# Performance work log

Hardware: AMD Instinct MI355X
Metric: run time of the kernel (lower is better)

Reference implementation:

```python
import jax, jax.numpy as jnp
import numpy as np
import math

N, Tp1, V = 256, 33, 10000
D_FEAT, H, W_DIM = 1280, 512, 256
NULL_IDX = 0


def setup_inputs() -> dict:
    key = jax.random.key(0)
    ks = jax.random.split(key, 10)
    feats = jax.random.normal(ks[0], (N, D_FEAT, 4, 4), dtype=jnp.float32)
    captions = jax.random.randint(ks[1], (N, Tp1), 0, V)
    W_proj = jax.random.normal(ks[2], (D_FEAT, H), dtype=jnp.float32) / math.sqrt(D_FEAT)
    b_proj = jnp.zeros((H,), dtype=jnp.float32)
    W_embed = jax.random.normal(ks[3], (V, W_DIM), dtype=jnp.float32) / math.sqrt(V)
    Wx = jax.random.normal(ks[4], (W_DIM, 4 * H), dtype=jnp.float32) / math.sqrt(W_DIM)
    Wh = jax.random.normal(ks[5], (H, 4 * H), dtype=jnp.float32) / math.sqrt(H)
    Wattn = jax.random.normal(ks[6], (H, 4 * H), dtype=jnp.float32) / math.sqrt(H)
    b = jnp.zeros((4 * H,), dtype=jnp.float32)
    W_vocab = jax.random.normal(ks[7], (H, V), dtype=jnp.float32) / math.sqrt(H)
    b_vocab = jnp.zeros((V,), dtype=jnp.float32)
    return {"feats": feats, "captions": captions, "W_proj": W_proj, "b_proj": b_proj,
            "W_embed": W_embed, "Wx": Wx, "Wh": Wh, "Wattn": Wattn, "b": b,
            "W_vocab": W_vocab, "b_vocab": b_vocab}


def _attention_lstm(x, A_flat, h0, Wx, Wh, Wattn, b):
    # x: (N,T,W), A_flat: (N,H,16), h0: (N,H)
    Hh = h0.shape[1]
    scale = 1.0 / math.sqrt(Hh)

    def step(carry, x_t):
        h, c = carry
        # scaled dot-product attention over the 16 spatial positions
        scores = jnp.einsum('nh,nhp->np', h, A_flat) * scale       # (N,16)
        w = jax.nn.softmax(scores, axis=1)
        attn = jnp.einsum('nhp,np->nh', A_flat, w)                 # (N,H)
        a = x_t @ Wx + h @ Wh + b + attn @ Wattn                   # (N,4H)
        i = jax.nn.sigmoid(a[:, 0:Hh])
        f = jax.nn.sigmoid(a[:, Hh:2 * Hh])
        o = jax.nn.sigmoid(a[:, 2 * Hh:3 * Hh])
        g = jnp.tanh(a[:, 3 * Hh:4 * Hh])
        c_next = f * c + i * g
        h_next = o * jnp.tanh(c_next)
        return (h_next, c_next), h_next

    (_, _), hs = jax.lax.scan(step, (h0, h0), jnp.swapaxes(x, 0, 1))
    return jnp.swapaxes(hs, 0, 1)  # (N,T,H)


def reference(feats, captions, W_proj, b_proj, W_embed, Wx, Wh, Wattn, b, W_vocab, b_vocab):
    cap_in = captions[:, :-1]   # (N,T)
    cap_out = captions[:, 1:]   # (N,T)
    # project CNN features per spatial location: (N,Dfeat,4,4) -> (N,H,4,4)
    A = jnp.einsum('ncij,ch->nhij', feats, W_proj) + b_proj[None, :, None, None]
    h0 = A.mean(axis=(2, 3))                     # (N,H); c0 = h0
    A_flat = A.reshape(A.shape[0], A.shape[1], 16)
    x = W_embed[cap_in]                           # (N,T,W)
    h = _attention_lstm(x, A_flat, h0, Wx, Wh, Wattn, b)
    scores = jnp.einsum('nth,hv->ntv', h, W_vocab) + b_vocab   # (N,T,V)
    # temporal softmax loss, sum over tokens (ignoring NULL), averaged over N
    logp = jax.nn.log_softmax(scores, axis=-1)
    nll = -jnp.take_along_axis(logp, cap_out[..., None], axis=-1)[..., 0]  # (N,T)
    mask = (cap_out != NULL_IDX).astype(scores.dtype)
    loss = jnp.sum(nll * mask) / scores.shape[0]
    return loss
```

## Files before the change

### kernel.cpp

```cpp
#include <hip/hip_runtime.h>
#include <hip/hip_bf16.h>

#define NB   256
#define NT   32
#define NV   10000
#define NVP  10240
#define NDF  1280
#define NH   512
#define VT_N 40

typedef short bf16x8 __attribute__((ext_vector_type(8)));
typedef float f32x4  __attribute__((ext_vector_type(4)));
typedef unsigned short u16;

__device__ __forceinline__ float b2f(u16 u) {
    union { unsigned i; float f; } v; v.i = ((unsigned)u) << 16; return v.f;
}
__device__ __forceinline__ u16 f2b(float f) {
    union { float f; unsigned i; } v; v.f = f;
    unsigned r = v.i + 0x7FFF + ((v.i >> 16) & 1);
    return (u16)(r >> 16);
}

__device__ __forceinline__ void gload16(const u16* g, u16* l) {
    __builtin_amdgcn_global_load_lds(
        (const __attribute__((address_space(1))) void*)g,
        (__attribute__((address_space(3))) void*)l, 16, 0, 0);
}

static const size_t B_C     = 0;
static const size_t B_SCP   = B_C     + (size_t)256*512*4;
static const size_t B_PMAX  = B_SCP   + (size_t)2*32*256*16*4;
static const size_t B_PSUM  = B_PMAX  + (size_t)8192*VT_N*4;
static const size_t B_TGT   = B_PSUM  + (size_t)8192*VT_N*4;
static const size_t B_LOSS  = B_TGT   + (size_t)8192*4;
static const size_t B_AB    = B_LOSS  + 16;
static const size_t B_XPB   = B_AB    + (size_t)256*16*512*2;
static const size_t B_HALLB = B_XPB   + (size_t)32*256*2048*2;
static const size_t B_WVT   = B_HALLB + (size_t)32*256*512*2;
static const size_t B_WXT   = B_WVT   + (size_t)10240*512*2;
static const size_t B_WHAT  = B_WXT   + (size_t)2048*256*2;
static const size_t B_HB0   = B_WHAT  + (size_t)2048*1024*2;
static const size_t B_HB1   = B_HB0   + (size_t)256*512*2;
static const size_t B_PREAW = B_HB1   + (size_t)256*512*2;

__global__ __launch_bounds__(256) void tconv_kernel(
    const float* __restrict__ src, u16* __restrict__ dst,
    int K, int N, int Npad, int ldK, int koff)
{
    __shared__ u16 tile[64][65];
    const int k0 = blockIdx.y * 64, n0 = blockIdx.x * 64, tid = threadIdx.x;
#pragma unroll
    for (int i = 0; i < 16; i++) {
        int idx = tid + i * 256;
        int kk = idx >> 6, nn = idx & 63;
        int n = n0 + nn;
        float v = (n < N) ? src[(size_t)(k0 + kk) * N + n] : 0.f;
        tile[kk][nn] = f2b(v);
    }
    __syncthreads();
#pragma unroll
    for (int i = 0; i < 16; i++) {
        int idx = tid + i * 256;
        int nn = idx >> 6, kk = idx & 63;
        int n = n0 + nn;
        if (n < Npad) dst[(size_t)n * ldK + koff + k0 + kk] = tile[kk][nn];
    }
}

__global__ __launch_bounds__(256) void ftrans_kernel(
    const float* __restrict__ feats, u16* __restrict__ fT)
{
    const int cch = blockIdx.x, n = blockIdx.y, tid = threadIdx.x;
    __shared__ u16 lt[64][17];
    const int c0 = cch * 64;
    const int c = tid >> 2, p4 = (tid & 3) * 4;
    float4 v = *(const float4*)(feats + (size_t)n * 20480 + (size_t)(c0 + c) * 16 + p4);
    lt[c][p4] = f2b(v.x); lt[c][p4 + 1] = f2b(v.y);
    lt[c][p4 + 2] = f2b(v.z); lt[c][p4 + 3] = f2b(v.w);
    __syncthreads();
    const int p = tid >> 4, cg = tid & 15;
    ushort4 o;
    o.x = lt[cg * 4 + 0][p]; o.y = lt[cg * 4 + 1][p];
    o.z = lt[cg * 4 + 2][p]; o.w = lt[cg * 4 + 3][p];
    *(ushort4*)(fT + (size_t)(n * 16 + p) * 1280 + c0 + cg * 4) = o;
}

__global__ __launch_bounds__(256) void proj_gemm_kernel(
    const u16* __restrict__ fT, const u16* __restrict__ WpT,
    const float* __restrict__ bp, u16* __restrict__ Ab)
{
    const int rt = blockIdx.x;
    const int tid = threadIdx.x, w = tid >> 6, lane = tid & 63;
    const int r0 = rt * 64;
    const int lm = lane & 15, lkq = lane >> 4, lk = lkq * 8;
    const int nbase = w * 128;

    f32x4 acc[4][8];
#pragma unroll
    for (int mt = 0; mt < 4; mt++)
#pragma unroll
        for (int nt = 0; nt < 8; nt++) acc[mt][nt] = (f32x4){0.f, 0.f, 0.f, 0.f};

    for (int kc = 0; kc < 1280; kc += 32) {
        bf16x8 af[4];
#pragma unroll
        for (int mt = 0; mt < 4; mt++)
            af[mt] = *(const bf16x8*)(fT + (size_t)(r0 + mt * 16 + lm) * 1280 + kc + lk);
#pragma unroll
        for (int nt = 0; nt < 8; nt++) {
            bf16x8 bfg = *(const bf16x8*)(WpT + (size_t)(nbase + nt * 16 + lm) * 1280 + kc + lk);
#pragma unroll
            for (int mt = 0; mt < 4; mt++)
                acc[mt][nt] = __builtin_amdgcn_mfma_f32_16x16x32_bf16(af[mt], bfg, acc[mt][nt], 0, 0, 0);
        }
    }
    float bbv[8];
#pragma unroll
    for (int nt = 0; nt < 8; nt++) bbv[nt] = bp[nbase + nt * 16 + lm];
#pragma unroll
    for (int mt = 0; mt < 4; mt++)
#pragma unroll
        for (int nt = 0; nt < 8; nt++)
#pragma unroll
            for (int r = 0; r < 4; r++) {
                int row = r0 + mt * 16 + lkq * 4 + r;
                int col = nbase + nt * 16 + lm;
                Ab[(size_t)row * 512 + col] = f2b(acc[mt][nt][r] + bbv[nt]);
            }
}

__global__ __launch_bounds__(256) void projmean_kernel(
    const u16* __restrict__ Ab, float* __restrict__ c0, u16* __restrict__ hb0)
{
    const int n = blockIdx.x, tid = threadIdx.x;
    const int col0 = tid, col1 = tid + 256;
    float s0 = 0.f, s1 = 0.f;
#pragma unroll
    for (int p = 0; p < 16; p++) {
        const u16* ap = Ab + ((size_t)n * 16 + p) * 512;
        s0 += b2f(ap[col0]);
        s1 += b2f(ap[col1]);
    }
    s0 *= 0.0625f; s1 *= 0.0625f;
    c0[n * 512 + col0] = s0;  c0[n * 512 + col1] = s1;
    hb0[(size_t)n * 512 + col0] = f2b(s0);
    hb0[(size_t)n * 512 + col1] = f2b(s1);
}

__global__ __launch_bounds__(256) void xp_mfma_kernel(
    const int* __restrict__ caps, const float* __restrict__ We,
    const u16* __restrict__ Wxt, const float* __restrict__ bb,
    u16* __restrict__ xpb)
{
    const int ct = blockIdx.x, rt = blockIdx.y;
    const int tid = threadIdx.x, w = tid >> 6, lane = tid & 63;
    const int r0 = rt * 64;
    const int lm = lane & 15, lkq = lane >> 4, lk = lkq * 8;
    const int nbase = ct * 512 + w * 128;

    int capm[4];
#pragma unroll
    for (int mt = 0; mt < 4; mt++) {
        int row = r0 + mt * 16 + lm;
        capm[mt] = caps[(row >> 5) * 33 + (row & 31)];
    }
    f32x4 acc[4][8];
#pragma unroll
    for (int mt = 0; mt < 4; mt++)
#pragma unroll
        for (int nt = 0; nt < 8; nt++) acc[mt][nt] = (f32x4){0.f, 0.f, 0.f, 0.f};

    for (int kc = 0; kc < 256; kc += 32) {
        bf16x8 af[4];
#pragma unroll
        for (int mt = 0; mt < 4; mt++) {
            const float* ap = We + (size_t)capm[mt] * 256 + kc + lk;
            float4 f0 = *(const float4*)ap;
            float4 f1 = *(const float4*)(ap + 4);
            bf16x8 t;
            t[0] = (short)f2b(f0.x); t[1] = (short)f2b(f0.y);
            t[2] = (short)f2b(f0.z); t[3] = (short)f2b(f0.w);
            t[4] = (short)f2b(f1.x); t[5] = (short)f2b(f1.y);
            t[6] = (short)f2b(f1.z); t[7] = (short)f2b(f1.w);
            af[mt] = t;
        }
#pragma unroll
        for (int nt = 0; nt < 8; nt++) {
            bf16x8 bfg = *(const bf16x8*)(Wxt + (size_t)(nbase + nt * 16 + lm) * 256 + kc + lk);
#pragma unroll
            for (int mt = 0; mt < 4; mt++)
                acc[mt][nt] = __builtin_amdgcn_mfma_f32_16x16x32_bf16(af[mt], bfg, acc[mt][nt], 0, 0, 0);
        }
    }
    float bbv[8];
#pragma unroll
    for (int nt = 0; nt < 8; nt++) bbv[nt] = bb[nbase + nt * 16 + lm];
#pragma unroll
    for (int mt = 0; mt < 4; mt++)
#pragma unroll
        for (int nt = 0; nt < 8; nt++)
#pragma unroll
            for (int r = 0; r < 4; r++) {
                int row = r0 + mt * 16 + lkq * 4 + r;
                int col = nbase + nt * 16 + lm;
                float v = acc[mt][nt][r] + bbv[nt];
                xpb[((size_t)(row & 31) * 256 + (row >> 5)) * 2048 + col] = f2b(v);
            }
}

__global__ __launch_bounds__(256) void preaw_mfma_kernel(
    const u16* __restrict__ Ab, const u16* __restrict__ what,
    u16* __restrict__ preaw)
{
    const int ct = blockIdx.x, rt = blockIdx.y;
    const int tid = threadIdx.x, w = tid >> 6, lane = tid & 63;
    const int r0 = rt * 64;
    const int lm = lane & 15, lkq = lane >> 4, lk = lkq * 8;
    const int nbase = ct * 512 + w * 128;

    f32x4 acc[4][8];
#pragma unroll
    for (int mt = 0; mt < 4; mt++)
#pragma unroll
        for (int nt = 0; nt < 8; nt++) acc[mt][nt] = (f32x4){0.f, 0.f, 0.f, 0.f};

    for (int kc = 0; kc < 512; kc += 32) {
        bf16x8 af[4];
#pragma unroll
        for (int mt = 0; mt < 4; mt++) {
            int row = r0 + mt * 16 + lm;
            af[mt] = *(const bf16x8*)(Ab + ((size_t)(row & 255) * 16 + (row >> 8)) * 512 + kc + lk);
        }
#pragma unroll
        for (int nt = 0; nt < 8; nt++) {
            bf16x8 bfg = *(const bf16x8*)(what + (size_t)(nbase + nt * 16 + lm) * 1024 + 512 + kc + lk);
#pragma unroll
            for (int mt = 0; mt < 4; mt++)
                acc[mt][nt] = __builtin_amdgcn_mfma_f32_16x16x32_bf16(af[mt], bfg, acc[mt][nt], 0, 0, 0);
        }
    }
#pragma unroll
    for (int mt = 0; mt < 4; mt++)
#pragma unroll
        for (int nt = 0; nt < 8; nt++)
#pragma unroll
            for (int r = 0; r < 4; r++) {
                int row = r0 + mt * 16 + lkq * 4 + r;
                int col = nbase + nt * 16 + lm;
                preaw[(size_t)row * 2048 + col] = f2b(acc[mt][nt][r]);
            }
}

__global__ __launch_bounds__(64) void score_init_kernel(
    const u16* __restrict__ hb0, const u16* __restrict__ Ab,
    float* __restrict__ scp)
{
    const int n = blockIdx.x, lane = threadIdx.x;
    const u16* hp = hb0 + (size_t)n * 512 + lane * 8;
    ushort4 h0 = *(const ushort4*)hp, h1 = *(const ushort4*)(hp + 4);
    float hv0 = b2f(h0.x), hv1 = b2f(h0.y), hv2 = b2f(h0.z), hv3 = b2f(h0.w);
    float hv4 = b2f(h1.x), hv5 = b2f(h1.y), hv6 = b2f(h1.z), hv7 = b2f(h1.w);
    float mine = 0.f;
#pragma unroll
    for (int p = 0; p < 16; p++) {
        const u16* ap = Ab + (size_t)n * 8192 + p * 512 + lane * 8;
        ushort4 a0 = *(const ushort4*)ap, a1 = *(const ushort4*)(ap + 4);
        float s = hv0*b2f(a0.x) + hv1*b2f(a0.y) + hv2*b2f(a0.z) + hv3*b2f(a0.w)
                + hv4*b2f(a1.x) + hv5*b2f(a1.y) + hv6*b2f(a1.z) + hv7*b2f(a1.w);
#pragma unroll
        for (int mask = 1; mask <= 32; mask <<= 1) s += __shfl_xor(s, mask, 64);
        if (lane == p) mine = s;
    }
    if (lane < 16) scp[n * 16 + lane] = mine;
    for (int i = lane; i < 31 * 16; i += 64)
        scp[(1 + (i >> 4)) * 4096 + n * 16 + (i & 15)] = 0.f;
}

__global__ __launch_bounds__(256) void gates_fused_kernel(
    const u16* __restrict__ hb_in, const float* __restrict__ scp_in,
    const u16* __restrict__ what, const u16* __restrict__ preaw,
    const u16* __restrict__ xpt, const u16* __restrict__ Ab,
    float* __restrict__ c, u16* __restrict__ hb_out,
    u16* __restrict__ hallbt, float* __restrict__ scp_out)
{
    const int rt = blockIdx.x, cg = blockIdx.y;
    const int tid = threadIdx.x, ty = tid >> 6, lane = tid & 63;
    const int lm = lane & 15, lkq = lane >> 4, lk = lkq * 8;
    const int r0 = rt * 16, hc0 = cg * 16;

    __shared__ u16 hs[16 * 520];
    __shared__ float sred[16][17];
    __shared__ float wts[16][17];
    __shared__ float gred[3][64][4];
    __shared__ u16 hnew[16][16];

#pragma unroll
    for (int i = 0; i < 8; i++) {
        int fid = tid + i * 256;
        int r = fid >> 7, c4 = fid & 127;
        *(ushort4*)&hs[r * 520 + c4 * 4] =
            *(const ushort4*)(hb_in + (size_t)(r0 + r) * 512 + c4 * 4);
    }
    {
        const int r = tid >> 4, p = tid & 15;
        float s = 0.f;
#pragma unroll
        for (int g = 0; g < 32; g++) s += scp_in[g * 4096 + (r0 + r) * 16 + p];
        sred[r][p] = s * 0.04419417382415922f;
    }
    __syncthreads();
    {
        const int r = tid >> 4, p = tid & 15;
        float m = -1e30f;
#pragma unroll
        for (int q = 0; q < 16; q++) m = fmaxf(m, sred[r][q]);
        float su = 0.f;
#pragma unroll
        for (int q = 0; q < 16; q++) su += __expf(sred[r][q] - m);
        wts[r][p] = __expf(sred[r][p] - m) / su;
    }
    __syncthreads();

    f32x4 acc = (f32x4){0.f, 0.f, 0.f, 0.f};
    const u16* brow = what + (size_t)(ty * 512 + hc0 + lm) * 1024 + lk;
    const u16* arow = &hs[lm * 520 + lk];
    for (int kc = 0; kc < 512; kc += 32) {
        bf16x8 af = *(const bf16x8*)(arow + kc);
        bf16x8 bfg = *(const bf16x8*)(brow + kc);
        acc = __builtin_amdgcn_mfma_f32_16x16x32_bf16(af, bfg, acc, 0, 0, 0);
    }
    float val[4];
#pragma unroll
    for (int r = 0; r < 4; r++) {
        const int rl = lkq * 4 + r, n = r0 + rl;
        const int col = ty * 512 + hc0 + lm;
        float s = acc[r] + b2f(xpt[(size_t)n * 2048 + col]);
#pragma unroll
        for (int p = 0; p < 16; p++)
            s += wts[rl][p] * b2f(preaw[((size_t)p * 256 + n) * 2048 + col]);
        val[r] = s;
    }
    if (ty > 0) {
#pragma unroll
        for (int r = 0; r < 4; r++) gred[ty - 1][lane][r] = val[r];
    }
    __syncthreads();
    if (ty == 0) {
#pragma unroll
        for (int r = 0; r < 4; r++) {
            const int rl = lkq * 4 + r, n = r0 + rl;
            const int hcol = hc0 + lm;
            float ai  = val[r];
            float af_ = gred[0][lane][r];
            float ao  = gred[1][lane][r];
            float ag  = gred[2][lane][r];
            float ig = 1.f / (1.f + __expf(-ai));
            float fg = 1.f / (1.f + __expf(-af_));
            float og = 1.f / (1.f + __expf(-ao));
            float gv = tanhf(ag);
            const int idx = n * 512 + hcol;
            float cn = fg * c[idx] + ig * gv;
            float hn = og * tanhf(cn);
            c[idx] = cn;
            u16 hbv = f2b(hn);
            hb_out[idx] = hbv;
            hallbt[idx] = hbv;
            hnew[rl][lm] = hbv;
        }
    }
    __syncthreads();
    {
        const int r = tid >> 4, p = tid & 15, n = r0 + r;
        const u16* ap = Ab + (size_t)n * 8192 + p * 512 + hc0;
        float s = 0.f;
#pragma unroll
        for (int j = 0; j < 16; j++) s += b2f(hnew[r][j]) * b2f(ap[j]);
        scp_out[cg * 4096 + n * 16 + p] = s;
    }
}

__global__ __launch_bounds__(512) void vocab_mfma_kernel(
    const u16* __restrict__ hallb, const u16* __restrict__ Wvt,
    const float* __restrict__ bv, const int* __restrict__ caps,
    float* __restrict__ pmax, float* __restrict__ psum, float* __restrict__ tgt)
{
    const int ct = blockIdx.x, rt = blockIdx.y;
    const int tid = threadIdx.x, w = tid >> 6, lane = tid & 63;
    const int wr = w >> 2, wc = w & 3;
    const int r0 = rt * 128, c0 = ct * 256;
    const int lm = lane & 15, lkq = lane >> 4;
    const int swz = lkq ^ ((lm >> 1) & 3);

    __shared__ u16 As[2][512 * 8];
    __shared__ u16 Bs[2][1024 * 8];
    __shared__ int tvs[128];
    __shared__ float cm[128][4], cs[128][4];

    if (tid < 128) {
        int row = r0 + tid;
        tvs[tid] = caps[(row & 255) * 33 + (row >> 8) + 1];
    }

    f32x4 acc[4][4];
#pragma unroll
    for (int mt = 0; mt < 4; mt++)
#pragma unroll
        for (int nt = 0; nt < 4; nt++) acc[mt][nt] = (f32x4){0.f, 0.f, 0.f, 0.f};

    const int sA = w * 64 + lane;
    const int rA = sA >> 2, kA = (sA & 3) ^ ((rA >> 1) & 3);
    const u16* gA = hallb + (size_t)(r0 + rA) * 512 + kA * 8;
    const int sB0 = w * 64 + lane, sB1 = sB0 + 512;
    const int cB0 = sB0 >> 2, kB0 = (sB0 & 3) ^ ((cB0 >> 1) & 3);
    const int cB1 = sB1 >> 2, kB1 = (sB1 & 3) ^ ((cB1 >> 1) & 3);
    const u16* gB0 = Wvt + (size_t)(c0 + cB0) * 512 + kB0 * 8;
    const u16* gB1 = Wvt + (size_t)(c0 + cB1) * 512 + kB1 * 8;

    auto stage = [&](int buf, int kc) {
        gload16(gA + kc, &As[buf][w * 512]);
        gload16(gB0 + kc, &Bs[buf][w * 512]);
        gload16(gB1 + kc, &Bs[buf][(w + 8) * 512]);
    };
    auto compute = [&](int buf) {
        bf16x8 af[4], bfr[4];
#pragma unroll
        for (int mt = 0; mt < 4; mt++)
            af[mt] = *(const bf16x8*)&As[buf][((wr * 64 + mt * 16 + lm) * 4 + swz) * 8];
#pragma unroll
        for (int nt = 0; nt < 4; nt++)
            bfr[nt] = *(const bf16x8*)&Bs[buf][((wc * 64 + nt * 16 + lm) * 4 + swz) * 8];
#pragma unroll
        for (int nt = 0; nt < 4; nt++)
#pragma unroll
            for (int mt = 0; mt < 4; mt++)
                acc[mt][nt] = __builtin_amdgcn_mfma_f32_16x16x32_bf16(af[mt], bfr[nt], acc[mt][nt], 0, 0, 0);
    };

    stage(0, 0);
#pragma unroll 1
    for (int t = 0; t < 15; ++t) {
        const int cur = t & 1;
        stage(cur ^ 1, (t + 1) * 32);
        asm volatile("s_waitcnt vmcnt(3)" ::: "memory");
        __builtin_amdgcn_s_barrier();
        compute(cur);
        __builtin_amdgcn_s_barrier();
    }
    asm volatile("s_waitcnt vmcnt(0)" ::: "memory");
    __builtin_amdgcn_s_barrier();
    compute(1);

    float bvv[4]; bool vld[4];
#pragma unroll
    for (int nt = 0; nt < 4; nt++) {
        int col = c0 + wc * 64 + nt * 16 + lm;
        vld[nt] = (col < NV);
        bvv[nt] = vld[nt] ? bv[col] : 0.f;
    }
#pragma unroll
    for (int mt = 0; mt < 4; mt++)
#pragma unroll
        for (int r = 0; r < 4; r++) {
            int rloc = wr * 64 + mt * 16 + lkq * 4 + r;
            int row = r0 + rloc;
            int tv = tvs[rloc];
            float vals[4]; float m = -1e30f;
#pragma unroll
            for (int nt = 0; nt < 4; nt++) {
                int col = c0 + wc * 64 + nt * 16 + lm;
                float v = vld[nt] ? (acc[mt][nt][r] + bvv[nt]) : -1e30f;
                vals[nt] = v;
                m = fmaxf(m, v);
                if (col == tv) tgt[row] = v;
            }
#pragma unroll
            for (int mask = 1; mask <= 8; mask <<= 1) m = fmaxf(m, __shfl_xor(m, mask, 64));
            float s = 0.f;
#pragma unroll
            for (int nt = 0; nt < 4; nt++) s += __expf(vals[nt] - m);
#pragma unroll
            for (int mask = 1; mask <= 8; mask <<= 1) s += __shfl_xor(s, mask, 64);
            if (lm == 0) { cm[rloc][wc] = m; cs[rloc][wc] = s; }
        }
    __syncthreads();
    if (tid < 128) {
        float M = -1e30f;
#pragma unroll
        for (int q = 0; q < 4; q++) M = fmaxf(M, cm[tid][q]);
        float S = 0.f;
#pragma unroll
        for (int q = 0; q < 4; q++) S += cs[tid][q] * __expf(cm[tid][q] - M);
        int row = r0 + tid;
        pmax[row * VT_N + ct] = M;
        psum[row * VT_N + ct] = S;
    }
}

__global__ __launch_bounds__(256) void loss_reduce_kernel(
    const float* __restrict__ pmax, const float* __restrict__ psum,
    const float* __restrict__ tgt, const int* __restrict__ caps,
    float* __restrict__ loss)
{
    const int row = blockIdx.x * 256 + threadIdx.x;
    float nll = 0.f;
    const int t = row >> 8, n = row & 255;
    const int tv = caps[n * 33 + t + 1];
    if (tv != 0) {
        float M = -1e30f;
#pragma unroll
        for (int vt = 0; vt < VT_N; vt++) M = fmaxf(M, pmax[row * VT_N + vt]);
        float S = 0.f;
#pragma unroll
        for (int vt = 0; vt < VT_N; vt++) S += psum[row * VT_N + vt] * __expf(pmax[row * VT_N + vt] - M);
        nll = logf(S) + M - tgt[row];
    }
#pragma unroll
    for (int off = 32; off; off >>= 1) nll += __shfl_down(nll, off, 64);
    __shared__ float r4[4];
    if ((threadIdx.x & 63) == 0) r4[threadIdx.x >> 6] = nll;
    __syncthreads();
    if (threadIdx.x == 0)
        atomicAdd(loss, (r4[0] + r4[1] + r4[2] + r4[3]) * (1.f / 256.f));
}

__global__ void finalize_kernel(const float* __restrict__ loss, float* __restrict__ out)
{
    if (threadIdx.x == 0 && blockIdx.x == 0) out[0] = loss[0];
}

extern "C" void kernel_launch(void* const* d_in, const int* in_sizes, int n_in,
                              void* d_out, int out_size, void* d_ws, size_t ws_size,
                              hipStream_t stream) {
    const float* feats = (const float*)d_in[0];
    const int*   caps  = (const int*)d_in[1];
    const float* Wp    = (const float*)d_in[2];
    const float* bp    = (const float*)d_in[3];
    const float* We    = (const float*)d_in[4];
    const float* Wx    = (const float*)d_in[5];
    const float* Wh    = (const float*)d_in[6];
    const float* Wattn = (const float*)d_in[7];
    const float* bb    = (const float*)d_in[8];
    const float* Wv    = (const float*)d_in[9];
    const float* bv    = (const float*)d_in[10];

    char* ws = (char*)d_ws;
    float* c     = (float*)(ws + B_C);
    float* scp0  = (float*)(ws + B_SCP);
    float* scp1  = scp0 + (size_t)32 * 4096;
    float* pmax  = (float*)(ws + B_PMAX);
    float* psum  = (float*)(ws + B_PSUM);
    float* tgt   = (float*)(ws + B_TGT);
    float* loss  = (float*)(ws + B_LOSS);
    u16*   Ab    = (u16*)(ws + B_AB);
    u16*   xpb   = (u16*)(ws + B_XPB);
    u16*   hallb = (u16*)(ws + B_HALLB);
    u16*   wvt   = (u16*)(ws + B_WVT);
    u16*   wxt   = (u16*)(ws + B_WXT);
    u16*   what  = (u16*)(ws + B_WHAT);
    u16*   hb[2] = { (u16*)(ws + B_HB0), (u16*)(ws + B_HB1) };
    u16*   preaw = (u16*)(ws + B_PREAW);
    u16*   fT    = wvt;
    u16*   WpT   = xpb;

    hipMemsetAsync(loss, 0, sizeof(float), stream);

    ftrans_kernel<<<dim3(20, 256), 256, 0, stream>>>(feats, fT);
    tconv_kernel<<<dim3(8, 20), 256, 0, stream>>>(Wp, WpT, 1280, 512, 512, 1280, 0);
    proj_gemm_kernel<<<64, 256, 0, stream>>>(fT, WpT, bp, Ab);
    projmean_kernel<<<256, 256, 0, stream>>>(Ab, c, hb[0]);

    tconv_kernel<<<dim3(160, 8), 256, 0, stream>>>(Wv, wvt, 512, NV, NVP, 512, 0);
    tconv_kernel<<<dim3(32, 4),  256, 0, stream>>>(Wx, wxt, 256, 2048, 2048, 256, 0);
    tconv_kernel<<<dim3(32, 8),  256, 0, stream>>>(Wh, what, 512, 2048, 2048, 1024, 0);
    tconv_kernel<<<dim3(32, 8),  256, 0, stream>>>(Wattn, what, 512, 2048, 2048, 1024, 512);
    xp_mfma_kernel<<<dim3(4, 128), 256, 0, stream>>>(caps, We, wxt, bb, xpb);
    preaw_mfma_kernel<<<dim3(4, 64), 256, 0, stream>>>(Ab, what, preaw);
    score_init_kernel<<<256, 64, 0, stream>>>(hb[0], Ab, scp0);

    for (int t = 0; t < NT; t++) {
        const int in = t & 1;
        gates_fused_kernel<<<dim3(16, 32), 256, 0, stream>>>(
            hb[in], in ? scp1 : scp0, what, preaw,
            xpb + (size_t)t * 524288, Ab, c,
            hb[1 - in], hallb + (size_t)t * 131072,
            in ? scp0 : scp1);
    }

    vocab_mfma_kernel<<<dim3(VT_N, 64), 512, 0, stream>>>(
        hallb, wvt, bv, caps, pmax, psum, tgt);
    loss_reduce_kernel<<<32, 256, 0, stream>>>(pmax, psum, tgt, caps, loss);
    finalize_kernel<<<1, 64, 0, stream>>>(loss, (float*)d_out);
}
```

Measured before the change: 883.5 us.

## Relayout preaw per sample, prefetch gate operands, widen proj GEMM grid

The attention-weight precompute now stores preaw so each sample's 16 spatial values for a column sit together, and writes them as vectorized ushort4. The per-step gates kernel loads its Wh fragments, preaw, xp, c and Ab slices into registers before the first barrier, overlapping global latency with the h tile load and softmax. The gate nonlinearity is also spread across all four waves instead of one. Separately, the projection GEMM grid is split across columns to use more CUs, at the cost of higher register pressure in the gates kernel (launch bounds set for two blocks per SM).

```diff
diff --git a/kernel.cpp b/kernel.cpp
--- a/kernel.cpp
+++ b/kernel.cpp
@@ -90,17 +90,17 @@
     const u16* __restrict__ fT, const u16* __restrict__ WpT,
     const float* __restrict__ bp, u16* __restrict__ Ab)
 {
-    const int rt = blockIdx.x;
+    const int ct = blockIdx.x, rt = blockIdx.y;
     const int tid = threadIdx.x, w = tid >> 6, lane = tid & 63;
     const int r0 = rt * 64;
     const int lm = lane & 15, lkq = lane >> 4, lk = lkq * 8;
-    const int nbase = w * 128;
-
-    f32x4 acc[4][8];
+    const int nbase = ct * 128 + w * 32;
+
+    f32x4 acc[4][2];
 #pragma unroll
     for (int mt = 0; mt < 4; mt++)
 #pragma unroll
-        for (int nt = 0; nt < 8; nt++) acc[mt][nt] = (f32x4){0.f, 0.f, 0.f, 0.f};
+        for (int nt = 0; nt < 2; nt++) acc[mt][nt] = (f32x4){0.f, 0.f, 0.f, 0.f};
 
     for (int kc = 0; kc < 1280; kc += 32) {
         bf16x8 af[4];
@@ -108,20 +108,20 @@
         for (int mt = 0; mt < 4; mt++)
             af[mt] = *(const bf16x8*)(fT + (size_t)(r0 + mt * 16 + lm) * 1280 + kc + lk);
 #pragma unroll
-        for (int nt = 0; nt < 8; nt++) {
+        for (int nt = 0; nt < 2; nt++) {
             bf16x8 bfg = *(const bf16x8*)(WpT + (size_t)(nbase + nt * 16 + lm) * 1280 + kc + lk);
 #pragma unroll
             for (int mt = 0; mt < 4; mt++)
                 acc[mt][nt] = __builtin_amdgcn_mfma_f32_16x16x32_bf16(af[mt], bfg, acc[mt][nt], 0, 0, 0);
         }
     }
-    float bbv[8];
-#pragma unroll
-    for (int nt = 0; nt < 8; nt++) bbv[nt] = bp[nbase + nt * 16 + lm];
+    float bbv[2];
+#pragma unroll
+    for (int nt = 0; nt < 2; nt++) bbv[nt] = bp[nbase + nt * 16 + lm];
 #pragma unroll
     for (int mt = 0; mt < 4; mt++)
 #pragma unroll
-        for (int nt = 0; nt < 8; nt++)
+        for (int nt = 0; nt < 2; nt++)
 #pragma unroll
             for (int r = 0; r < 4; r++) {
                 int row = r0 + mt * 16 + lkq * 4 + r;
@@ -228,10 +228,8 @@
     for (int kc = 0; kc < 512; kc += 32) {
         bf16x8 af[4];
 #pragma unroll
-        for (int mt = 0; mt < 4; mt++) {
-            int row = r0 + mt * 16 + lm;
-            af[mt] = *(const bf16x8*)(Ab + ((size_t)(row & 255) * 16 + (row >> 8)) * 512 + kc + lk);
-        }
+        for (int mt = 0; mt < 4; mt++)
+            af[mt] = *(const bf16x8*)(Ab + (size_t)(r0 + mt * 16 + lm) * 512 + kc + lk);
 #pragma unroll
         for (int nt = 0; nt < 8; nt++) {
             bf16x8 bfg = *(const bf16x8*)(what + (size_t)(nbase + nt * 16 + lm) * 1024 + 512 + kc + lk);
@@ -241,15 +239,17 @@
         }
     }
 #pragma unroll
-    for (int mt = 0; mt < 4; mt++)
-#pragma unroll
-        for (int nt = 0; nt < 8; nt++)
-#pragma unroll
-            for (int r = 0; r < 4; r++) {
-                int row = r0 + mt * 16 + lkq * 4 + r;
-                int col = nbase + nt * 16 + lm;
-                preaw[(size_t)row * 2048 + col] = f2b(acc[mt][nt][r]);
-            }
+    for (int mt = 0; mt < 4; mt++) {
+        int nIdx = (r0 >> 4) + mt;
+#pragma unroll
+        for (int nt = 0; nt < 8; nt++) {
+            int col = nbase + nt * 16 + lm;
+            ushort4 o;
+            o.x = f2b(acc[mt][nt][0]); o.y = f2b(acc[mt][nt][1]);
+            o.z = f2b(acc[mt][nt][2]); o.w = f2b(acc[mt][nt][3]);
+            *(ushort4*)(preaw + (size_t)nIdx * 32768 + (size_t)col * 16 + lkq * 4) = o;
+        }
+    }
 }
 
 __global__ __launch_bounds__(64) void score_init_kernel(
@@ -277,7 +277,7 @@
         scp[(1 + (i >> 4)) * 4096 + n * 16 + (i & 15)] = 0.f;
 }
 
-__global__ __launch_bounds__(256) void gates_fused_kernel(
+__global__ __launch_bounds__(256, 2) void gates_fused_kernel(
     const u16* __restrict__ hb_in, const float* __restrict__ scp_in,
     const u16* __restrict__ what, const u16* __restrict__ preaw,
     const u16* __restrict__ xpt, const u16* __restrict__ Ab,
@@ -292,91 +292,112 @@
     __shared__ u16 hs[16 * 520];
     __shared__ float sred[16][17];
     __shared__ float wts[16][17];
-    __shared__ float gred[3][64][4];
+    __shared__ float gred[4][16][18];
     __shared__ u16 hnew[16][16];
+
+    const int col = ty * 512 + hc0 + lm;
+
+    const u16* brow = what + (size_t)col * 1024 + lk;
+    bf16x8 bfa[16];
+#pragma unroll
+    for (int i = 0; i < 16; i++) bfa[i] = *(const bf16x8*)(brow + i * 32);
+
+    ushort4 pwv[4][4];
+#pragma unroll
+    for (int r = 0; r < 4; r++) {
+        const u16* pp = preaw + (size_t)(r0 + lkq * 4 + r) * 32768 + (size_t)col * 16;
+#pragma unroll
+        for (int j = 0; j < 4; j++) pwv[r][j] = *(const ushort4*)(pp + j * 4);
+    }
+    u16 xpw[4];
+#pragma unroll
+    for (int r = 0; r < 4; r++) xpw[r] = xpt[(size_t)(r0 + lkq * 4 + r) * 2048 + col];
+
+    const int rg = lkq * 4 + ty;
+    const int idxg = (r0 + rg) * 512 + hc0 + lm;
+    float cin = c[idxg];
+
+    const int rs = tid >> 4, ps = tid & 15;
+    ushort4 abv[4];
+    {
+        const u16* ap = Ab + (size_t)(r0 + rs) * 8192 + ps * 512 + hc0;
+#pragma unroll
+        for (int j = 0; j < 4; j++) abv[j] = *(const ushort4*)(ap + j * 4);
+    }
 
 #pragma unroll
     for (int i = 0; i < 8; i++) {
         int fid = tid + i * 256;
-        int r = fid >> 7, c4 = fid & 127;
-        *(ushort4*)&hs[r * 520 + c4 * 4] =
-            *(const ushort4*)(hb_in + (size_t)(r0 + r) * 512 + c4 * 4);
+        int rr = fid >> 7, c4 = fid & 127;
+        *(ushort4*)&hs[rr * 520 + c4 * 4] =
+            *(const ushort4*)(hb_in + (size_t)(r0 + rr) * 512 + c4 * 4);
     }
     {
-        const int r = tid >> 4, p = tid & 15;
         float s = 0.f;
 #pragma unroll
-        for (int g = 0; g < 32; g++) s += scp_in[g * 4096 + (r0 + r) * 16 + p];
-        sred[r][p] = s * 0.04419417382415922f;
+        for (int g = 0; g < 32; g++) s += scp_in[g * 4096 + (r0 + rs) * 16 + ps];
+        sred[rs][ps] = s * 0.04419417382415922f;
     }
     __syncthreads();
     {
-        const int r = tid >> 4, p = tid & 15;
         float m = -1e30f;
 #pragma unroll
-        for (int q = 0; q < 16; q++) m = fmaxf(m, sred[r][q]);
+        for (int q = 0; q < 16; q++) m = fmaxf(m, sred[rs][q]);
         float su = 0.f;
 #pragma unroll
-        for (int q = 0; q < 16; q++) su += __expf(sred[r][q] - m);
-        wts[r][p] = __expf(sred[r][p] - m) / su;
-    }
-    __syncthreads();
-
+        for (int q = 0; q < 16; q++) su += __expf(sred[rs][q] - m);
+        wts[rs][ps] = __expf(sred[rs][ps] - m) / su;
+    }
     f32x4 acc = (f32x4){0.f, 0.f, 0.f, 0.f};
-    const u16* brow = what + (size_t)(ty * 512 + hc0 + lm) * 1024 + lk;
     const u16* arow = &hs[lm * 520 + lk];
-    for (int kc = 0; kc < 512; kc += 32) {
-        bf16x8 af = *(const bf16x8*)(arow + kc);
-        bf16x8 bfg = *(const bf16x8*)(brow + kc);
-        acc = __builtin_amdgcn_mfma_f32_16x16x32_bf16(af, bfg, acc, 0, 0, 0);
-    }
-    float val[4];
+#pragma unroll
+    for (int i = 0; i < 16; i++) {
+        bf16x8 af = *(const bf16x8*)(arow + i * 32);
+        acc = __builtin_amdgcn_mfma_f32_16x16x32_bf16(af, bfa[i], acc, 0, 0, 0);
+    }
+    __syncthreads();
 #pragma unroll
     for (int r = 0; r < 4; r++) {
-        const int rl = lkq * 4 + r, n = r0 + rl;
-        const int col = ty * 512 + hc0 + lm;
-        float s = acc[r] + b2f(xpt[(size_t)n * 2048 + col]);
-#pragma unroll
-        for (int p = 0; p < 16; p++)
-            s += wts[rl][p] * b2f(preaw[((size_t)p * 256 + n) * 2048 + col]);
-        val[r] = s;
-    }
-    if (ty > 0) {
-#pragma unroll
-        for (int r = 0; r < 4; r++) gred[ty - 1][lane][r] = val[r];
-    }
-    __syncthreads();
-    if (ty == 0) {
-#pragma unroll
-        for (int r = 0; r < 4; r++) {
-            const int rl = lkq * 4 + r, n = r0 + rl;
-            const int hcol = hc0 + lm;
-            float ai  = val[r];
-            float af_ = gred[0][lane][r];
-            float ao  = gred[1][lane][r];
-            float ag  = gred[2][lane][r];
-            float ig = 1.f / (1.f + __expf(-ai));
-            float fg = 1.f / (1.f + __expf(-af_));
-            float og = 1.f / (1.f + __expf(-ao));
-            float gv = tanhf(ag);
-            const int idx = n * 512 + hcol;
-            float cn = fg * c[idx] + ig * gv;
-            float hn = og * tanhf(cn);
-            c[idx] = cn;
-            u16 hbv = f2b(hn);
-            hb_out[idx] = hbv;
-            hallbt[idx] = hbv;
-            hnew[rl][lm] = hbv;
-        }
+        const int rl = lkq * 4 + r;
+        float s = acc[r] + b2f(xpw[r]);
+#pragma unroll
+        for (int j = 0; j < 4; j++) {
+            s += wts[rl][j * 4 + 0] * b2f(pwv[r][j].x);
+            s += wts[rl][j * 4 + 1] * b2f(pwv[r][j].y);
+            s += wts[rl][j * 4 + 2] * b2f(pwv[r][j].z);
+            s += wts[rl][j * 4 + 3] * b2f(pwv[r][j].w);
+        }
+        gred[ty][rl][lm] = s;
     }
     __syncthreads();
     {
-        const int r = tid >> 4, p = tid & 15, n = r0 + r;
-        const u16* ap = Ab + (size_t)n * 8192 + p * 512 + hc0;
+        float ai  = gred[0][rg][lm];
+        float af_ = gred[1][rg][lm];
+        float ao  = gred[2][rg][lm];
+        float ag  = gred[3][rg][lm];
+        float ig = 1.f / (1.f + __expf(-ai));
+        float fg = 1.f / (1.f + __expf(-af_));
+        float og = 1.f / (1.f + __expf(-ao));
+        float gv = tanhf(ag);
+        float cn = fg * cin + ig * gv;
+        float hn = og * tanhf(cn);
+        c[idxg] = cn;
+        u16 hbv = f2b(hn);
+        hb_out[idxg] = hbv;
+        hallbt[idxg] = hbv;
+        hnew[rg][lm] = hbv;
+    }
+    __syncthreads();
+    {
         float s = 0.f;
 #pragma unroll
-        for (int j = 0; j < 16; j++) s += b2f(hnew[r][j]) * b2f(ap[j]);
-        scp_out[cg * 4096 + n * 16 + p] = s;
+        for (int j = 0; j < 4; j++) {
+            s += b2f(hnew[rs][j * 4 + 0]) * b2f(abv[j].x);
+            s += b2f(hnew[rs][j * 4 + 1]) * b2f(abv[j].y);
+            s += b2f(hnew[rs][j * 4 + 2]) * b2f(abv[j].z);
+            s += b2f(hnew[rs][j * 4 + 3]) * b2f(abv[j].w);
+        }
+        scp_out[cg * 4096 + (r0 + rs) * 16 + ps] = s;
     }
 }
 
@@ -567,7 +588,7 @@
 
     ftrans_kernel<<<dim3(20, 256), 256, 0, stream>>>(feats, fT);
     tconv_kernel<<<dim3(8, 20), 256, 0, stream>>>(Wp, WpT, 1280, 512, 512, 1280, 0);
-    proj_gemm_kernel<<<64, 256, 0, stream>>>(fT, WpT, bp, Ab);
+    proj_gemm_kernel<<<dim3(4, 64), 256, 0, stream>>>(fT, WpT, bp, Ab);
     projmean_kernel<<<256, 256, 0, stream>>>(Ab, c, hb[0]);
 
     tconv_kernel<<<dim3(160, 8), 256, 0, stream>>>(Wv, wvt, 512, NV, NVP, 512, 0);
```

After: 744.9 us, median of 2. 1.19x faster.
